# Performance work log

Measured on AMD Instinct MI355X. Metric: run time of the kernel, lower is better.

## Reference

```python
import jax, jax.numpy as jnp
import numpy as np
from jax import lax

ROUNDS = 64
HIDDEN = 256
BATCH = 16384


def setup_inputs() -> dict:
    key = jax.random.key(0)
    k1, k2, k3 = jax.random.split(key, 3)
    # state: (B, 256) bits in {0,1} as float32 (output of bytes_to_bits)
    state = jax.random.bernoulli(k1, 0.5, (BATCH, HIDDEN)).astype(jnp.float32)
    # matrices: (64, 256, 256) ternary values in {-1,0,1} (byte % 3 - 1)
    matrices = jax.random.randint(k2, (ROUNDS, HIDDEN, HIDDEN), -1, 2).astype(jnp.float32)
    # noise: (B, 64, 256) bits in {0,1} derived from sha256 of the nonce
    noise = jax.random.bernoulli(k3, 0.5, (BATCH, ROUNDS, HIDDEN)).astype(jnp.float32)
    return {"state": state, "matrices": matrices, "noise": noise}


def reference(state, matrices, noise):
    # 64-round recurrence: s <- (floor(s @ M_r^T + n_r)) mod 2
    noise_r = jnp.transpose(noise, (1, 0, 2))  # (R, B, H)

    def step(s, xs):
        M, n = xs  # M: (H,H), n: (B,H)
        s = jnp.remainder(jnp.floor(s @ M.T + n), 2.0)
        return s, None

    final, _ = lax.scan(step, state, (matrices, noise_r))
    return final  # (B, 256) bits as float32
```

## Files before the change

kernel.cpp:

```cpp
#include <hip/hip_runtime.h>

typedef unsigned int u32;
typedef unsigned long long u64;

#define R_ROUNDS 64
#define HID 256
#define BATCH 16384
#define RPW 4


__global__ __launch_bounds__(256) void pack_matrices_kernel(
        const float* __restrict__ M, u32* __restrict__ P) {
    const int lane = threadIdx.x & 63;
    const int row  = (int)((blockIdx.x * blockDim.x + threadIdx.x) >> 6);
    const float4 v = *(const float4*)(M + (size_t)row * HID + 4 * lane);
    const u64 b0 = __ballot(v.x != 0.0f);
    const u64 b1 = __ballot(v.y != 0.0f);
    const u64 b2 = __ballot(v.z != 0.0f);
    const u64 b3 = __ballot(v.w != 0.0f);
    if (lane < 8) {
        const int i = lane >> 1;
        u64 bb = b0;
        if (i == 1) bb = b1;
        if (i == 2) bb = b2;
        if (i == 3) bb = b3;
        P[row * 8 + lane] = (lane & 1) ? (u32)(bb >> 32) : (u32)bb;
    }
}

__global__ __launch_bounds__(256, 4) void tenshash_kernel(
        const float* __restrict__ state,
        const u32*  __restrict__ pA,
        const float* __restrict__ noise,
        float* __restrict__ out) {
    const int lane = threadIdx.x & 63;
    const int warp = threadIdx.x >> 6;
    const int wave = (int)(blockIdx.x * 4 + warp);
    const int row0 = wave * RPW;

    __shared__ u32 smem[2][2048];

    u64 S0[RPW], S1[RPW], S2[RPW], S3[RPW];
#pragma unroll
    for (int rw = 0; rw < RPW; ++rw) {
        const float4 v = *(const float4*)(state + (size_t)(row0 + rw) * HID + 4 * lane);
        S0[rw] = __ballot(v.x != 0.0f);
        S1[rw] = __ballot(v.y != 0.0f);
        S2[rw] = __ballot(v.z != 0.0f);
        S3[rw] = __ballot(v.w != 0.0f);
    }

    const float* no_l = noise + (size_t)row0 * (R_ROUNDS * HID) + 4 * lane;

    const int sa = lane >> 3, sb = lane & 7;
    const int src_chunk_lo = (sa << 3) + (sb ^ sa);
    auto STAGE = [&](int r, int b) {
        if (warp == 0) {
            const char* g = (const char*)(pA + (size_t)r * 2048);
#pragma unroll
            for (int t = 0; t < 8; ++t) {
                __builtin_amdgcn_global_load_lds(
                    (const __attribute__((address_space(1))) void*)
                        (g + t * 1024 + src_chunk_lo * 16),
                    (__attribute__((address_space(3))) void*)&smem[b][t * 256],
                    16, 0, 0);
            }
        }
    };
    auto LOADN = [&](float4* n, int r) {
#pragma unroll
        for (int rw = 0; rw < RPW; ++rw)
            n[rw] = *(const float4*)(no_l + (size_t)rw * (R_ROUNDS * HID) + r * HID);
    };
    auto RUN = [&](int b, const float4* n) {
        const uint4* p = (const uint4*)&smem[b][0];
        uint4 a[8];
#pragma unroll
        for (int t = 0; t < 8; ++t)
            a[t] = p[(lane << 3) + (t ^ (lane & 7))];
#pragma unroll
        for (int rw = 0; rw < RPW; ++rw) {
            u64 ns0, ns1, ns2, ns3;
#pragma unroll
            for (int i = 0; i < 4; ++i) {
                const u64 W0 = (u64)a[2 * i].x     | ((u64)a[2 * i].y     << 32);
                const u64 W1 = (u64)a[2 * i].z     | ((u64)a[2 * i].w     << 32);
                const u64 W2 = (u64)a[2 * i + 1].x | ((u64)a[2 * i + 1].y << 32);
                const u64 W3 = (u64)a[2 * i + 1].z | ((u64)a[2 * i + 1].w << 32);
                const float nfv = (i == 0) ? n[rw].x : (i == 1) ? n[rw].y
                                : (i == 2) ? n[rw].z : n[rw].w;
                const u32 c = (u32)__popcll(W0 & S0[rw]) + (u32)__popcll(W1 & S1[rw])
                            + (u32)__popcll(W2 & S2[rw]) + (u32)__popcll(W3 & S3[rw])
                            + (u32)nfv;
                const u64 nb = __ballot((c & 1u) != 0);
                if (i == 0) ns0 = nb; else if (i == 1) ns1 = nb;
                else if (i == 2) ns2 = nb; else ns3 = nb;
            }
            S0[rw] = ns0; S1[rw] = ns1; S2[rw] = ns2; S3[rw] = ns3;
        }
    };

    float4 nA[RPW], nB[RPW];
    STAGE(0, 0);
    LOADN(nA, 0);
    __syncthreads();
#pragma unroll 1
    for (int r = 0; r < R_ROUNDS; r += 2) {
        STAGE(r + 1, 1);
        LOADN(nB, r + 1);
        RUN(0, nA);
        __syncthreads();
        if (r + 2 < R_ROUNDS) {
            STAGE(r + 2, 0);
            LOADN(nA, r + 2);
        }
        RUN(1, nB);
        __syncthreads();
    }

#pragma unroll
    for (int rw = 0; rw < RPW; ++rw) {
        float4 o;
        o.x = (float)((u32)(S0[rw] >> lane) & 1u);
        o.y = (float)((u32)(S1[rw] >> lane) & 1u);
        o.z = (float)((u32)(S2[rw] >> lane) & 1u);
        o.w = (float)((u32)(S3[rw] >> lane) & 1u);
        *(float4*)(out + (size_t)(row0 + rw) * HID + 4 * lane) = o;
    }
}

extern "C" void kernel_launch(void* const* d_in, const int* in_sizes, int n_in,
                              void* d_out, int out_size, void* d_ws, size_t ws_size,
                              hipStream_t stream) {
    const float* state = (const float*)d_in[0];
    const float* mats  = (const float*)d_in[1];
    const float* noise = (const float*)d_in[2];
    float* out         = (float*)d_out;
    u32* pA            = (u32*)d_ws;

    pack_matrices_kernel<<<(R_ROUNDS * HID) / 4, 256, 0, stream>>>(mats, pA);

    const int blocks = (BATCH / RPW) / 4;
    tenshash_kernel<<<blocks, 256, 0, stream>>>(state, pA, noise, out);
}
```

Before: 230.6 us.

## Pre-permute packed matrices for conflict-free LDS reads and split staging across waves

The pack kernel now writes matrix bits in a permuted layout so each lane's eight 16-byte chunks sit at stride 64, which lets the per-round LDS read use a plain lane-contiguous index without the XOR swizzle. The async global-to-LDS staging is spread across all four waves (two chunks each) instead of wave 0 issuing all eight, and the noise loads are issued before the staging. This aims to balance the issue load and simplify addressing. Any change in LDS bank behaviour depends on the new layout, and the order swap may shift how load latency overlaps with compute.

```diff
diff --git a/kernel.cpp b/kernel.cpp
--- a/kernel.cpp
+++ b/kernel.cpp
@@ -12,19 +12,23 @@
 __global__ __launch_bounds__(256) void pack_matrices_kernel(
         const float* __restrict__ M, u32* __restrict__ P) {
     const int lane = threadIdx.x & 63;
-    const int row  = (int)((blockIdx.x * blockDim.x + threadIdx.x) >> 6);
-    const float4 v = *(const float4*)(M + (size_t)row * HID + 4 * lane);
+    const int gw   = (int)((blockIdx.x * blockDim.x + threadIdx.x) >> 6);
+    const int r    = gw >> 8;
+    const int jj   = gw & 255;
+    const float4 v = *(const float4*)(M + (size_t)gw * HID + 4 * lane);
     const u64 b0 = __ballot(v.x != 0.0f);
     const u64 b1 = __ballot(v.y != 0.0f);
     const u64 b2 = __ballot(v.z != 0.0f);
     const u64 b3 = __ballot(v.w != 0.0f);
     if (lane < 8) {
-        const int i = lane >> 1;
+        const int w = lane;
         u64 bb = b0;
-        if (i == 1) bb = b1;
-        if (i == 2) bb = b2;
-        if (i == 3) bb = b3;
-        P[row * 8 + lane] = (lane & 1) ? (u32)(bb >> 32) : (u32)bb;
+        if ((w >> 1) == 1) bb = b1;
+        if ((w >> 1) == 2) bb = b2;
+        if ((w >> 1) == 3) bb = b3;
+        const u32 val = (w & 1) ? (u32)(bb >> 32) : (u32)bb;
+        const int t = 2 * (jj & 3) + (w >> 2);
+        P[r * 2048 + t * 256 + (jj >> 2) * 4 + (w & 3)] = val;
     }
 }
 
@@ -52,19 +56,15 @@
 
     const float* no_l = noise + (size_t)row0 * (R_ROUNDS * HID) + 4 * lane;
 
-    const int sa = lane >> 3, sb = lane & 7;
-    const int src_chunk_lo = (sa << 3) + (sb ^ sa);
     auto STAGE = [&](int r, int b) {
-        if (warp == 0) {
-            const char* g = (const char*)(pA + (size_t)r * 2048);
+        const char* g = (const char*)(pA + (size_t)r * 2048);
 #pragma unroll
-            for (int t = 0; t < 8; ++t) {
-                __builtin_amdgcn_global_load_lds(
-                    (const __attribute__((address_space(1))) void*)
-                        (g + t * 1024 + src_chunk_lo * 16),
-                    (__attribute__((address_space(3))) void*)&smem[b][t * 256],
-                    16, 0, 0);
-            }
+        for (int t = 2 * warp; t < 2 * warp + 2; ++t) {
+            __builtin_amdgcn_global_load_lds(
+                (const __attribute__((address_space(1))) void*)
+                    (g + t * 1024 + lane * 16),
+                (__attribute__((address_space(3))) void*)&smem[b][t * 256],
+                16, 0, 0);
         }
     };
     auto LOADN = [&](float4* n, int r) {
@@ -72,12 +72,12 @@
         for (int rw = 0; rw < RPW; ++rw)
             n[rw] = *(const float4*)(no_l + (size_t)rw * (R_ROUNDS * HID) + r * HID);
     };
-    auto RUN = [&](int b, const float4* n) {
-        const uint4* p = (const uint4*)&smem[b][0];
+    auto RUN = [&](const u32* base, const float4* n) {
+        const uint4* p = (const uint4*)base;
         uint4 a[8];
 #pragma unroll
         for (int t = 0; t < 8; ++t)
-            a[t] = p[(lane << 3) + (t ^ (lane & 7))];
+            a[t] = p[(t << 6) + lane];
 #pragma unroll
         for (int rw = 0; rw < RPW; ++rw) {
             u64 ns0, ns1, ns2, ns3;
@@ -101,20 +101,21 @@
     };
 
     float4 nA[RPW], nB[RPW];
+
+    LOADN(nA, 0);
     STAGE(0, 0);
-    LOADN(nA, 0);
     __syncthreads();
 #pragma unroll 1
     for (int r = 0; r < R_ROUNDS; r += 2) {
+        LOADN(nB, r + 1);
         STAGE(r + 1, 1);
-        LOADN(nB, r + 1);
-        RUN(0, nA);
+        RUN(&smem[0][0], nA);
         __syncthreads();
         if (r + 2 < R_ROUNDS) {
+            LOADN(nA, r + 2);
             STAGE(r + 2, 0);
-            LOADN(nA, r + 2);
         }
-        RUN(1, nB);
+        RUN(&smem[1][0], nB);
         __syncthreads();
     }
 
```

Measured after the change: 234.4 us. About the same (+1.7%).
